# Kernel optimization log

Hardware: AMD Instinct MI355X
Metric: run time of the kernel (lower is better)

## Reference

```python
import jax, jax.numpy as jnp
import numpy as np

N_NODES = 50000
N_EDGES = 800000
F_IN = 128
F_OUT = 128


def gcn_conv(x, W, b, src, tgt, w, n):
    # x: [n, F_in]; GCNConv with add_self_loops=True, improved=False (fill=1.0)
    lin = x @ W  # [n, F_out]
    deg = jax.ops.segment_sum(w, tgt, num_segments=n) + 1.0  # self-loop weight 1
    dinv = jax.lax.rsqrt(deg)
    normw = dinv[src] * w * dinv[tgt]  # [E]
    agg = jax.ops.segment_sum(lin[src] * normw[:, None], tgt, num_segments=n)
    return agg + lin * (dinv * dinv)[:, None] + b


def setup_inputs() -> dict:
    key = jax.random.key(0)
    ks = jax.random.split(key, 16)
    X = jax.random.normal(ks[0], (1, N_NODES, F_IN), jnp.float32)
    edge_index = jax.random.randint(ks[1], (2, N_EDGES), 0, N_NODES, jnp.int64)
    edge_weight = jax.random.uniform(ks[2], (N_EDGES,), jnp.float32)
    H = jax.random.normal(ks[3], (1, N_NODES, F_OUT), jnp.float32)
    s = 1.0 / np.sqrt(F_IN)
    s2 = 1.0 / np.sqrt(2 * F_OUT)
    params = {
        'W_z': jax.random.uniform(ks[4], (F_IN, F_OUT), jnp.float32, -s, s),
        'b_z': jnp.zeros((F_OUT,), jnp.float32),
        'W_r': jax.random.uniform(ks[5], (F_IN, F_OUT), jnp.float32, -s, s),
        'b_r': jnp.zeros((F_OUT,), jnp.float32),
        'W_h': jax.random.uniform(ks[6], (F_IN, F_OUT), jnp.float32, -s, s),
        'b_h': jnp.zeros((F_OUT,), jnp.float32),
        'Wl_z': jax.random.uniform(ks[7], (2 * F_OUT, F_OUT), jnp.float32, -s2, s2),
        'bl_z': jax.random.uniform(ks[8], (F_OUT,), jnp.float32, -s2, s2),
        'Wl_r': jax.random.uniform(ks[9], (2 * F_OUT, F_OUT), jnp.float32, -s2, s2),
        'bl_r': jax.random.uniform(ks[10], (F_OUT,), jnp.float32, -s2, s2),
        'Wl_h': jax.random.uniform(ks[11], (2 * F_OUT, F_OUT), jnp.float32, -s2, s2),
        'bl_h': jax.random.uniform(ks[12], (F_OUT,), jnp.float32, -s2, s2),
    }
    return dict(X=X, edge_index=edge_index, edge_weight=edge_weight, H=H, **params)


def reference(X, edge_index, edge_weight, H,
              W_z, b_z, W_r, b_r, W_h, b_h,
              Wl_z, bl_z, Wl_r, bl_r, Wl_h, bl_h):
    B, N, _ = X.shape
    n = B * N
    x = X.reshape(n, -1)
    src, tgt = edge_index[0], edge_index[1]

    cz = gcn_conv(x, W_z, b_z, src, tgt, edge_weight, n).reshape(B, N, -1)
    Z = jax.nn.sigmoid(jnp.concatenate([cz, H], axis=2) @ Wl_z + bl_z)

    cr = gcn_conv(x, W_r, b_r, src, tgt, edge_weight, n).reshape(B, N, -1)
    R = jax.nn.sigmoid(jnp.concatenate([cr, H], axis=2) @ Wl_r + bl_r)

    ch = gcn_conv(x, W_h, b_h, src, tgt, edge_weight, n).reshape(B, N, -1)
    H_tilde = jnp.tanh(jnp.concatenate([ch, H * R], axis=2) @ Wl_h + bl_h)

    return Z * H + (1.0 - Z) * H_tilde
```

## Files before the change

kernel.cpp:

```cpp
#include <hip/hip_runtime.h>
#include <hip/hip_bf16.h>

#define N_NODES 50000
#define N_EDGES 800000
#define M_PAD   50048
#define NBLK5   1564
#define CAP     96

typedef __attribute__((ext_vector_type(8))) short bf16x8_t;
typedef __attribute__((ext_vector_type(4))) float f32x4_t;
typedef __attribute__((ext_vector_type(2))) float f32x2_t;

__device__ __forceinline__ unsigned short f2bf(float f) {
    unsigned u = __float_as_uint(f);
    u += 0x7FFFu + ((u >> 16) & 1u);
    return (unsigned short)(u >> 16);
}
__device__ __forceinline__ float bf2f(unsigned short h) {
    return __uint_as_float(((unsigned)h) << 16);
}


__global__ void prep1_kernel(const float* __restrict__ Wz, const float* __restrict__ Wr,
                             const float* __restrict__ Wh,
                             const float* __restrict__ bz, const float* __restrict__ br,
                             const float* __restrict__ bh,
                             const float* __restrict__ Wlz, const float* __restrict__ Wlr,
                             const float* __restrict__ Wlh,
                             const float* __restrict__ blz, const float* __restrict__ blr,
                             const float* __restrict__ blh,
                             float* __restrict__ Pf, float* __restrict__ cg,
                             int* __restrict__ counts) {
    int tid = blockIdx.x * 256 + threadIdx.x;
    if (tid < N_NODES) counts[tid] = 0;
    if (tid < 3 * 16384) {
        int g = tid / 16384, k = (tid / 128) % 128, n = tid & 127;
        const float* W  = (g == 0) ? Wz  : (g == 1) ? Wr  : Wh;
        const float* Wl = (g == 0) ? Wlz : (g == 1) ? Wlr : Wlh;
        float acc = 0.f;
        #pragma unroll 8
        for (int j = 0; j < 128; ++j)
            acc = fmaf(W[k * 128 + j], Wl[j * 128 + n], acc);
        Pf[tid] = acc;
    } else if (tid < 3 * 16384 + 384) {
        int u = tid - 3 * 16384;
        int g = u / 128, n = u & 127;
        const float* b  = (g == 0) ? bz  : (g == 1) ? br  : bh;
        const float* Wl = (g == 0) ? Wlz : (g == 1) ? Wlr : Wlh;
        const float* bl = (g == 0) ? blz : (g == 1) ? blr : blh;
        float acc = bl[n];
        #pragma unroll 8
        for (int j = 0; j < 128; ++j)
            acc = fmaf(b[j], Wl[j * 128 + n], acc);
        cg[u] = acc;
    }
}

__global__ void wfrag2_kernel(const float* __restrict__ Pf,
                              const float* __restrict__ Wlz, const float* __restrict__ Wlr,
                              const float* __restrict__ Wlh,
                              unsigned short* __restrict__ Wf2) {
    int tid = blockIdx.x * 256 + threadIdx.x;
    if (tid >= 6 * 2048) return;
    int m = tid / 2048, t = tid % 2048;
    int nt = t / 256, ks = (t / 64) % 4, lane = t % 64;
    const float* src;
    if (m < 3) src = Pf + m * 16384;
    else       src = ((m == 3) ? Wlz : (m == 4) ? Wlr : Wlh) + 128 * 128;
    unsigned short* dst = Wf2 + m * 16384 + ((nt * 4 + ks) * 64 + lane) * 8;
    int n = nt * 16 + (lane & 15);
    int k0 = ks * 32 + 8 * (lane >> 4);
    #pragma unroll
    for (int j = 0; j < 8; ++j) dst[j] = f2bf(src[(k0 + j) * 128 + n]);
}

__global__ void place_kernel(const int* __restrict__ EI, const float* __restrict__ EW,
                             int* __restrict__ counts, int2* __restrict__ rec,
                             const float* __restrict__ Hf, unsigned short* __restrict__ Hb) {
    int i = blockIdx.x * 256 + threadIdx.x;
    if (i < N_NODES * 32) {
        float4 h = ((const float4*)Hf)[i];
        ushort4 b;
        b.x = f2bf(h.x); b.y = f2bf(h.y); b.z = f2bf(h.z); b.w = f2bf(h.w);
        ((ushort4*)Hb)[i] = b;
    }
    if (i < N_EDGES) {
        int s = EI[i];
        int t = EI[N_EDGES + i];
        int pos = atomicAdd(&counts[t], 1);
        if (pos < CAP) rec[(size_t)t * CAP + pos] = make_int2(s, __float_as_int(EW[i]));
    }
}

__global__ void degconv_kernel(const int* __restrict__ counts, const int2* __restrict__ rec,
                               const float* __restrict__ X,
                               float* __restrict__ dinv, unsigned* __restrict__ Xf) {
    int tid = blockIdx.x * 256 + threadIdx.x;
    int node = tid >> 4;
    int j = tid & 15;
    if (node >= N_NODES) return;
    int c = counts[node]; c = (c < CAP) ? c : CAP;
    const int2* rb = rec + (size_t)node * CAP;
    float d = 0.f;
    for (int e = j; e < c; e += 16) d += __int_as_float(rb[e].y);
    d += __shfl_xor(d, 8, 16);
    d += __shfl_xor(d, 4, 16);
    d += __shfl_xor(d, 2, 16);
    d += __shfl_xor(d, 1, 16);
    d += 1.0f;
    float di = rsqrtf(d);
    if (j == 0) dinv[node] = di;
    float4 xa = *(const float4*)(X + (size_t)node * 128 + j * 8);
    float4 xb = *(const float4*)(X + (size_t)node * 128 + j * 8 + 4);
    float s0 = di * xa.x, s1 = di * xa.y, s2 = di * xa.z, s3 = di * xa.w;
    float s4 = di * xb.x, s5 = di * xb.y, s6 = di * xb.z, s7 = di * xb.w;
    int u0 = __builtin_amdgcn_cvt_pk_fp8_f32(s0, s1, 0, false);
    u0 = __builtin_amdgcn_cvt_pk_fp8_f32(s2, s3, u0, true);
    int u1 = __builtin_amdgcn_cvt_pk_fp8_f32(s4, s5, 0, false);
    u1 = __builtin_amdgcn_cvt_pk_fp8_f32(s6, s7, u1, true);
    uint2 o;
    o.x = (unsigned)u0; o.y = (unsigned)u1;
    *(uint2*)(Xf + (size_t)node * 32 + j * 2) = o;
}


__global__ __launch_bounds__(512) void fused_kernel(const unsigned* __restrict__ Xf,
                                                    const unsigned short* __restrict__ Hb,
                                                    const float* __restrict__ dinv,
                                                    const int* __restrict__ counts,
                                                    const int2* __restrict__ rec,
                                                    const unsigned short* __restrict__ Wf2,
                                                    const float* __restrict__ cg,
                                                    float* __restrict__ out) {
    __shared__ unsigned short ys[32][136];
    __shared__ unsigned short hs[32][136];
    __shared__ unsigned short rls[32][136];
    int tid = threadIdx.x;
    int wave = tid >> 6, lane = tid & 63;
    int rowbase = blockIdx.x * 32;
    int rlo = lane & 15;
    int kg = 8 * (lane >> 4);
    int n0 = wave;

    {
        int r = tid >> 4, co = (tid & 15) * 8;
        int row = rowbase + r;
        bf16x8_t h;
        if (row < N_NODES) h = *(const bf16x8_t*)(Hb + (size_t)row * 128 + co);
        else {
            #pragma unroll
            for (int j = 0; j < 8; ++j) h[j] = 0;
        }
        *(bf16x8_t*)(&hs[r][co]) = h;
    }

    {
        int nl = wave * 4 + (lane >> 4);
        int half = (lane >> 3) & 1;
        int lg = lane & 7;
        int node = rowbase + nl;
        float acc[16];
        #pragma unroll
        for (int j = 0; j < 16; ++j) acc[j] = 0.f;
        float dt = 0.f;
        if (node < N_NODES) {
            dt = dinv[node];
            if (half == 0) {
                uint4 xs = *(const uint4*)(Xf + (size_t)node * 32 + lg * 4);
                #pragma unroll
                for (int k = 0; k < 4; ++k) {
                    unsigned u = ((const unsigned*)&xs)[k];
                    f32x2_t lo = __builtin_amdgcn_cvt_pk_f32_fp8((int)u, false);
                    f32x2_t hi = __builtin_amdgcn_cvt_pk_f32_fp8((int)u, true);
                    acc[k * 4 + 0] = lo[0];
                    acc[k * 4 + 1] = lo[1];
                    acc[k * 4 + 2] = hi[0];
                    acc[k * 4 + 3] = hi[1];
                }
            }
            int c = counts[node]; c = (c < CAP) ? c : CAP;
            const int2* rb = rec + (size_t)node * CAP;
            int e = half;
            int2 r;
            uint4 xa;
            float wcur = 0.f;
            if (e < c) {
                r = rb[e];
                xa = *(const uint4*)(Xf + (size_t)r.x * 32 + lg * 4);
                wcur = __int_as_float(r.y);
                if (e + 2 < c) r = rb[e + 2];
            }
            while (e < c) {
                uint4 xn;
                float wn = 0.f;
                int en = e + 2;
                if (en < c) {
                    xn = *(const uint4*)(Xf + (size_t)r.x * 32 + lg * 4);
                    wn = __int_as_float(r.y);
                    if (en + 2 < c) r = rb[en + 2];
                }
                #pragma unroll
                for (int k = 0; k < 4; ++k) {
                    unsigned u = ((const unsigned*)&xa)[k];
                    f32x2_t lo = __builtin_amdgcn_cvt_pk_f32_fp8((int)u, false);
                    f32x2_t hi = __builtin_amdgcn_cvt_pk_f32_fp8((int)u, true);
                    acc[k * 4 + 0] = fmaf(wcur, lo[0], acc[k * 4 + 0]);
                    acc[k * 4 + 1] = fmaf(wcur, lo[1], acc[k * 4 + 1]);
                    acc[k * 4 + 2] = fmaf(wcur, hi[0], acc[k * 4 + 2]);
                    acc[k * 4 + 3] = fmaf(wcur, hi[1], acc[k * 4 + 3]);
                }
                xa = xn; wcur = wn;
                e = en;
            }
        }
        #pragma unroll
        for (int j = 0; j < 16; ++j) acc[j] += __shfl_xor(acc[j], 8, 64);
        if (half == 0) {
            ushort4 o0, o1, o2, o3;
            o0.x = f2bf(dt * acc[0]);  o0.y = f2bf(dt * acc[1]);
            o0.z = f2bf(dt * acc[2]);  o0.w = f2bf(dt * acc[3]);
            o1.x = f2bf(dt * acc[4]);  o1.y = f2bf(dt * acc[5]);
            o1.z = f2bf(dt * acc[6]);  o1.w = f2bf(dt * acc[7]);
            o2.x = f2bf(dt * acc[8]);  o2.y = f2bf(dt * acc[9]);
            o2.z = f2bf(dt * acc[10]); o2.w = f2bf(dt * acc[11]);
            o3.x = f2bf(dt * acc[12]); o3.y = f2bf(dt * acc[13]);
            o3.z = f2bf(dt * acc[14]); o3.w = f2bf(dt * acc[15]);
            *(ushort4*)(&ys[nl][lg * 16])      = o0;
            *(ushort4*)(&ys[nl][lg * 16 + 4])  = o1;
            *(ushort4*)(&ys[nl][lg * 16 + 8])  = o2;
            *(ushort4*)(&ys[nl][lg * 16 + 12]) = o3;
        }
    }
    __syncthreads();

    const unsigned short* Az = Wf2;
    const unsigned short* Ar = Wf2 + 16384;
    const unsigned short* Ah = Wf2 + 2 * 16384;
    const unsigned short* Bz = Wf2 + 3 * 16384;
    const unsigned short* Br = Wf2 + 4 * 16384;
    const unsigned short* Bh = Wf2 + 5 * 16384;
    int col = n0 * 16 + rlo;

    {
        f32x4_t a0 = f32x4_t{0.f, 0.f, 0.f, 0.f};
        f32x4_t a1 = f32x4_t{0.f, 0.f, 0.f, 0.f};
        #pragma unroll
        for (int ks = 0; ks < 4; ++ks) {
            bf16x8_t y0 = *(const bf16x8_t*)(&ys[rlo][ks * 32 + kg]);
            bf16x8_t y1 = *(const bf16x8_t*)(&ys[16 + rlo][ks * 32 + kg]);
            bf16x8_t b = *(const bf16x8_t*)(Ar + ((n0 * 4 + ks) * 64 + lane) * 8);
            a0 = __builtin_amdgcn_mfma_f32_16x16x32_bf16(y0, b, a0, 0, 0, 0);
            a1 = __builtin_amdgcn_mfma_f32_16x16x32_bf16(y1, b, a1, 0, 0, 0);
        }
        #pragma unroll
        for (int ks = 0; ks < 4; ++ks) {
            bf16x8_t h0 = *(const bf16x8_t*)(&hs[rlo][ks * 32 + kg]);
            bf16x8_t h1 = *(const bf16x8_t*)(&hs[16 + rlo][ks * 32 + kg]);
            bf16x8_t b = *(const bf16x8_t*)(Br + ((n0 * 4 + ks) * 64 + lane) * 8);
            a0 = __builtin_amdgcn_mfma_f32_16x16x32_bf16(h0, b, a0, 0, 0, 0);
            a1 = __builtin_amdgcn_mfma_f32_16x16x32_bf16(h1, b, a1, 0, 0, 0);
        }
        float crv = cg[128 + col];
        #pragma unroll
        for (int r = 0; r < 4; ++r) {
            float p0 = a0[r] + crv;
            float p1 = a1[r] + crv;
            rls[4 * (lane >> 4) + r][col] = f2bf(1.0f / (1.0f + __expf(-p0)));
            rls[16 + 4 * (lane >> 4) + r][col] = f2bf(1.0f / (1.0f + __expf(-p1)));
        }
    }
    __syncthreads();

    {
        f32x4_t az0 = f32x4_t{0.f, 0.f, 0.f, 0.f};
        f32x4_t az1 = f32x4_t{0.f, 0.f, 0.f, 0.f};
        f32x4_t at0 = f32x4_t{0.f, 0.f, 0.f, 0.f};
        f32x4_t at1 = f32x4_t{0.f, 0.f, 0.f, 0.f};
        #pragma unroll
        for (int ks = 0; ks < 4; ++ks) {
            bf16x8_t y0 = *(const bf16x8_t*)(&ys[rlo][ks * 32 + kg]);
            bf16x8_t y1 = *(const bf16x8_t*)(&ys[16 + rlo][ks * 32 + kg]);
            bf16x8_t bz_ = *(const bf16x8_t*)(Az + ((n0 * 4 + ks) * 64 + lane) * 8);
            bf16x8_t bh_ = *(const bf16x8_t*)(Ah + ((n0 * 4 + ks) * 64 + lane) * 8);
            az0 = __builtin_amdgcn_mfma_f32_16x16x32_bf16(y0, bz_, az0, 0, 0, 0);
            az1 = __builtin_amdgcn_mfma_f32_16x16x32_bf16(y1, bz_, az1, 0, 0, 0);
            at0 = __builtin_amdgcn_mfma_f32_16x16x32_bf16(y0, bh_, at0, 0, 0, 0);
            at1 = __builtin_amdgcn_mfma_f32_16x16x32_bf16(y1, bh_, at1, 0, 0, 0);
        }
        #pragma unroll
        for (int ks = 0; ks < 4; ++ks) {
            bf16x8_t h0 = *(const bf16x8_t*)(&hs[rlo][ks * 32 + kg]);
            bf16x8_t h1 = *(const bf16x8_t*)(&hs[16 + rlo][ks * 32 + kg]);
            bf16x8_t rf0 = *(const bf16x8_t*)(&rls[rlo][ks * 32 + kg]);
            bf16x8_t rf1 = *(const bf16x8_t*)(&rls[16 + rlo][ks * 32 + kg]);
            bf16x8_t hr0, hr1;
            #pragma unroll
            for (int j = 0; j < 8; ++j) {
                hr0[j] = (short)f2bf(bf2f((unsigned short)h0[j]) * bf2f((unsigned short)rf0[j]));
                hr1[j] = (short)f2bf(bf2f((unsigned short)h1[j]) * bf2f((unsigned short)rf1[j]));
            }
            bf16x8_t bz_ = *(const bf16x8_t*)(Bz + ((n0 * 4 + ks) * 64 + lane) * 8);
            bf16x8_t bh_ = *(const bf16x8_t*)(Bh + ((n0 * 4 + ks) * 64 + lane) * 8);
            az0 = __builtin_amdgcn_mfma_f32_16x16x32_bf16(h0, bz_, az0, 0, 0, 0);
            az1 = __builtin_amdgcn_mfma_f32_16x16x32_bf16(h1, bz_, az1, 0, 0, 0);
            at0 = __builtin_amdgcn_mfma_f32_16x16x32_bf16(hr0, bh_, at0, 0, 0, 0);
            at1 = __builtin_amdgcn_mfma_f32_16x16x32_bf16(hr1, bh_, at1, 0, 0, 0);
        }
        float czv = cg[col];
        float chv = cg[256 + col];
        #pragma unroll
        for (int rt = 0; rt < 2; ++rt) {
            #pragma unroll
            for (int r = 0; r < 4; ++r) {
                int rl = rt * 16 + 4 * (lane >> 4) + r;
                int row = rowbase + rl;
                if (row < N_NODES) {
                    float pz = (rt == 0 ? az0[r] : az1[r]) + czv;
                    float z = 1.0f / (1.0f + __expf(-pz));
                    float ph = (rt == 0 ? at0[r] : at1[r]) + chv;
                    float t = __expf(-2.0f * fabsf(ph));
                    float th = (1.0f - t) / (1.0f + t);
                    th = copysignf(th, ph);
                    float h = bf2f(hs[rl][col]);
                    out[(size_t)row * 128 + col] = z * h + (1.0f - z) * th;
                }
            }
        }
    }
}


extern "C" void kernel_launch(void* const* d_in, const int* in_sizes, int n_in,
                              void* d_out, int out_size, void* d_ws, size_t ws_size,
                              hipStream_t stream) {
    const float*      X   = (const float*)d_in[0];
    const int*        EI  = (const int*)d_in[1];
    const float*      EW  = (const float*)d_in[2];
    const float*      Hf  = (const float*)d_in[3];
    const float*      Wz  = (const float*)d_in[4];
    const float*      bz  = (const float*)d_in[5];
    const float*      Wr  = (const float*)d_in[6];
    const float*      br  = (const float*)d_in[7];
    const float*      Wh  = (const float*)d_in[8];
    const float*      bh  = (const float*)d_in[9];
    const float*      Wlz = (const float*)d_in[10];
    const float*      blz = (const float*)d_in[11];
    const float*      Wlr = (const float*)d_in[12];
    const float*      blr = (const float*)d_in[13];
    const float*      Wlh = (const float*)d_in[14];
    const float*      blh = (const float*)d_in[15];
    float* out = (float*)d_out;

    char* p = (char*)d_ws;
    auto alloc = [&](size_t bytes) {
        char* r = p;
        p += (bytes + 255) & ~(size_t)255;
        return r;
    };
    int*   counts = (int*)alloc(M_PAD * 4);
    float* dinv   = (float*)alloc(M_PAD * 4);
    int2*  rec    = (int2*)alloc((size_t)N_NODES * CAP * 8);
    unsigned*       Xf  = (unsigned*)alloc((size_t)M_PAD * 128);
    unsigned short* Hb  = (unsigned short*)alloc((size_t)M_PAD * 128 * 2);
    float* Pf  = (float*)alloc(3 * 128 * 128 * 4);
    float* cgb = (float*)alloc(3 * 128 * 4);
    unsigned short* Wf2 = (unsigned short*)alloc(6 * 128 * 128 * 2);

    prep1_kernel<<<196, 256, 0, stream>>>(Wz, Wr, Wh, bz, br, bh,
                                          Wlz, Wlr, Wlh, blz, blr, blh,
                                          Pf, cgb, counts);
    wfrag2_kernel<<<48, 256, 0, stream>>>(Pf, Wlz, Wlr, Wlh, Wf2);
    place_kernel<<<6250, 256, 0, stream>>>(EI, EW, counts, rec, Hf, Hb);
    degconv_kernel<<<3125, 256, 0, stream>>>(counts, rec, X, dinv, Xf);
    fused_kernel<<<NBLK5, 512, 0, stream>>>(Xf, Hb, dinv, counts, rec, Wf2, cgb, out);
}
```

Baseline: 124.0 us.

## Double fused kernel block to 1024 threads, four lane groups per node gather

The fused GCN-GRU kernel now runs 1024 threads per block. Each node's edge gather is split across four 8-lane groups instead of two, and the groups are combined with two xor-shuffles. In the MFMA stage each wave handles one 16-row tile instead of two, which halves per-wave accumulator and register use. The aim is more memory-level parallelism in the gather, which dominates the kernel. The cost is more shuffle reduction work and redundant weight-fragment loads, since the B fragments are now fetched by twice as many waves.

```diff
diff --git a/kernel.cpp b/kernel.cpp
--- a/kernel.cpp
+++ b/kernel.cpp
@@ -124,14 +124,14 @@
 }
 
 
-__global__ __launch_bounds__(512) void fused_kernel(const unsigned* __restrict__ Xf,
-                                                    const unsigned short* __restrict__ Hb,
-                                                    const float* __restrict__ dinv,
-                                                    const int* __restrict__ counts,
-                                                    const int2* __restrict__ rec,
-                                                    const unsigned short* __restrict__ Wf2,
-                                                    const float* __restrict__ cg,
-                                                    float* __restrict__ out) {
+__global__ __launch_bounds__(1024) void fused_kernel(const unsigned* __restrict__ Xf,
+                                                     const unsigned short* __restrict__ Hb,
+                                                     const float* __restrict__ dinv,
+                                                     const int* __restrict__ counts,
+                                                     const int2* __restrict__ rec,
+                                                     const unsigned short* __restrict__ Wf2,
+                                                     const float* __restrict__ cg,
+                                                     float* __restrict__ out) {
     __shared__ unsigned short ys[32][136];
     __shared__ unsigned short hs[32][136];
     __shared__ unsigned short rls[32][136];
@@ -140,23 +140,21 @@
     int rowbase = blockIdx.x * 32;
     int rlo = lane & 15;
     int kg = 8 * (lane >> 4);
-    int n0 = wave;
+    int n0 = wave & 7;
+    int rt = wave >> 3;
 
     {
-        int r = tid >> 4, co = (tid & 15) * 8;
+        int r = tid >> 5, co = (tid & 31) * 4;
         int row = rowbase + r;
-        bf16x8_t h;
-        if (row < N_NODES) h = *(const bf16x8_t*)(Hb + (size_t)row * 128 + co);
-        else {
-            #pragma unroll
-            for (int j = 0; j < 8; ++j) h[j] = 0;
-        }
-        *(bf16x8_t*)(&hs[r][co]) = h;
+        ushort4 h;
+        if (row < N_NODES) h = *(const ushort4*)(Hb + (size_t)row * 128 + co);
+        else { h.x = 0; h.y = 0; h.z = 0; h.w = 0; }
+        *(ushort4*)(&hs[r][co]) = h;
     }
 
     {
-        int nl = wave * 4 + (lane >> 4);
-        int half = (lane >> 3) & 1;
+        int nl = 2 * wave + (lane >> 5);
+        int grp = (lane >> 3) & 3;
         int lg = lane & 7;
         int node = rowbase + nl;
         float acc[16];
@@ -165,7 +163,7 @@
         float dt = 0.f;
         if (node < N_NODES) {
             dt = dinv[node];
-            if (half == 0) {
+            if (grp == 0) {
                 uint4 xs = *(const uint4*)(Xf + (size_t)node * 32 + lg * 4);
                 #pragma unroll
                 for (int k = 0; k < 4; ++k) {
@@ -180,7 +178,7 @@
             }
             int c = counts[node]; c = (c < CAP) ? c : CAP;
             const int2* rb = rec + (size_t)node * CAP;
-            int e = half;
+            int e = grp;
             int2 r;
             uint4 xa;
             float wcur = 0.f;
@@ -188,16 +186,16 @@
                 r = rb[e];
                 xa = *(const uint4*)(Xf + (size_t)r.x * 32 + lg * 4);
                 wcur = __int_as_float(r.y);
-                if (e + 2 < c) r = rb[e + 2];
+                if (e + 4 < c) r = rb[e + 4];
             }
             while (e < c) {
                 uint4 xn;
                 float wn = 0.f;
-                int en = e + 2;
+                int en = e + 4;
                 if (en < c) {
                     xn = *(const uint4*)(Xf + (size_t)r.x * 32 + lg * 4);
                     wn = __int_as_float(r.y);
-                    if (en + 2 < c) r = rb[en + 2];
+                    if (en + 4 < c) r = rb[en + 4];
                 }
                 #pragma unroll
                 for (int k = 0; k < 4; ++k) {
@@ -214,8 +212,13 @@
             }
         }
         #pragma unroll
-        for (int j = 0; j < 16; ++j) acc[j] += __shfl_xor(acc[j], 8, 64);
-        if (half == 0) {
+        for (int j = 0; j < 16; ++j) {
+            float v = acc[j];
+            v += __shfl_xor(v, 8, 64);
+            v += __shfl_xor(v, 16, 64);
+            acc[j] = v;
+        }
+        if (grp == 0) {
             ushort4 o0, o1, o2, o3;
             o0.x = f2bf(dt * acc[0]);  o0.y = f2bf(dt * acc[1]);
             o0.z = f2bf(dt * acc[2]);  o0.w = f2bf(dt * acc[3]);
@@ -240,90 +243,70 @@
     const unsigned short* Br = Wf2 + 4 * 16384;
     const unsigned short* Bh = Wf2 + 5 * 16384;
     int col = n0 * 16 + rlo;
+    int yrow = rt * 16 + rlo;
 
     {
-        f32x4_t a0 = f32x4_t{0.f, 0.f, 0.f, 0.f};
-        f32x4_t a1 = f32x4_t{0.f, 0.f, 0.f, 0.f};
+        f32x4_t a = f32x4_t{0.f, 0.f, 0.f, 0.f};
         #pragma unroll
         for (int ks = 0; ks < 4; ++ks) {
-            bf16x8_t y0 = *(const bf16x8_t*)(&ys[rlo][ks * 32 + kg]);
-            bf16x8_t y1 = *(const bf16x8_t*)(&ys[16 + rlo][ks * 32 + kg]);
+            bf16x8_t y = *(const bf16x8_t*)(&ys[yrow][ks * 32 + kg]);
             bf16x8_t b = *(const bf16x8_t*)(Ar + ((n0 * 4 + ks) * 64 + lane) * 8);
-            a0 = __builtin_amdgcn_mfma_f32_16x16x32_bf16(y0, b, a0, 0, 0, 0);
-            a1 = __builtin_amdgcn_mfma_f32_16x16x32_bf16(y1, b, a1, 0, 0, 0);
+            a = __builtin_amdgcn_mfma_f32_16x16x32_bf16(y, b, a, 0, 0, 0);
         }
         #pragma unroll
         for (int ks = 0; ks < 4; ++ks) {
-            bf16x8_t h0 = *(const bf16x8_t*)(&hs[rlo][ks * 32 + kg]);
-            bf16x8_t h1 = *(const bf16x8_t*)(&hs[16 + rlo][ks * 32 + kg]);
+            bf16x8_t h = *(const bf16x8_t*)(&hs[yrow][ks * 32 + kg]);
             bf16x8_t b = *(const bf16x8_t*)(Br + ((n0 * 4 + ks) * 64 + lane) * 8);
-            a0 = __builtin_amdgcn_mfma_f32_16x16x32_bf16(h0, b, a0, 0, 0, 0);
-            a1 = __builtin_amdgcn_mfma_f32_16x16x32_bf16(h1, b, a1, 0, 0, 0);
+            a = __builtin_amdgcn_mfma_f32_16x16x32_bf16(h, b, a, 0, 0, 0);
         }
         float crv = cg[128 + col];
         #pragma unroll
         for (int r = 0; r < 4; ++r) {
-            float p0 = a0[r] + crv;
-            float p1 = a1[r] + crv;
-            rls[4 * (lane >> 4) + r][col] = f2bf(1.0f / (1.0f + __expf(-p0)));
-            rls[16 + 4 * (lane >> 4) + r][col] = f2bf(1.0f / (1.0f + __expf(-p1)));
+            float pv = a[r] + crv;
+            rls[rt * 16 + 4 * (lane >> 4) + r][col] = f2bf(1.0f / (1.0f + __expf(-pv)));
         }
     }
     __syncthreads();
 
     {
-        f32x4_t az0 = f32x4_t{0.f, 0.f, 0.f, 0.f};
-        f32x4_t az1 = f32x4_t{0.f, 0.f, 0.f, 0.f};
-        f32x4_t at0 = f32x4_t{0.f, 0.f, 0.f, 0.f};
-        f32x4_t at1 = f32x4_t{0.f, 0.f, 0.f, 0.f};
+        f32x4_t az = f32x4_t{0.f, 0.f, 0.f, 0.f};
+        f32x4_t at = f32x4_t{0.f, 0.f, 0.f, 0.f};
         #pragma unroll
         for (int ks = 0; ks < 4; ++ks) {
-            bf16x8_t y0 = *(const bf16x8_t*)(&ys[rlo][ks * 32 + kg]);
-            bf16x8_t y1 = *(const bf16x8_t*)(&ys[16 + rlo][ks * 32 + kg]);
+            bf16x8_t y = *(const bf16x8_t*)(&ys[yrow][ks * 32 + kg]);
             bf16x8_t bz_ = *(const bf16x8_t*)(Az + ((n0 * 4 + ks) * 64 + lane) * 8);
             bf16x8_t bh_ = *(const bf16x8_t*)(Ah + ((n0 * 4 + ks) * 64 + lane) * 8);
-            az0 = __builtin_amdgcn_mfma_f32_16x16x32_bf16(y0, bz_, az0, 0, 0, 0);
-            az1 = __builtin_amdgcn_mfma_f32_16x16x32_bf16(y1, bz_, az1, 0, 0, 0);
-            at0 = __builtin_amdgcn_mfma_f32_16x16x32_bf16(y0, bh_, at0, 0, 0, 0);
-            at1 = __builtin_amdgcn_mfma_f32_16x16x32_bf16(y1, bh_, at1, 0, 0, 0);
+            az = __builtin_amdgcn_mfma_f32_16x16x32_bf16(y, bz_, az, 0, 0, 0);
+            at = __builtin_amdgcn_mfma_f32_16x16x32_bf16(y, bh_, at, 0, 0, 0);
         }
         #pragma unroll
         for (int ks = 0; ks < 4; ++ks) {
-            bf16x8_t h0 = *(const bf16x8_t*)(&hs[rlo][ks * 32 + kg]);
-            bf16x8_t h1 = *(const bf16x8_t*)(&hs[16 + rlo][ks * 32 + kg]);
-            bf16x8_t rf0 = *(const bf16x8_t*)(&rls[rlo][ks * 32 + kg]);
-            bf16x8_t rf1 = *(const bf16x8_t*)(&rls[16 + rlo][ks * 32 + kg]);
-            bf16x8_t hr0, hr1;
+            bf16x8_t h = *(const bf16x8_t*)(&hs[yrow][ks * 32 + kg]);
+            bf16x8_t rf = *(const bf16x8_t*)(&rls[yrow][ks * 32 + kg]);
+            bf16x8_t hr;
             #pragma unroll
-            for (int j = 0; j < 8; ++j) {
-                hr0[j] = (short)f2bf(bf2f((unsigned short)h0[j]) * bf2f((unsigned short)rf0[j]));
-                hr1[j] = (short)f2bf(bf2f((unsigned short)h1[j]) * bf2f((unsigned short)rf1[j]));
-            }
+            for (int j = 0; j < 8; ++j)
+                hr[j] = (short)f2bf(bf2f((unsigned short)h[j]) * bf2f((unsigned short)rf[j]));
             bf16x8_t bz_ = *(const bf16x8_t*)(Bz + ((n0 * 4 + ks) * 64 + lane) * 8);
             bf16x8_t bh_ = *(const bf16x8_t*)(Bh + ((n0 * 4 + ks) * 64 + lane) * 8);
-            az0 = __builtin_amdgcn_mfma_f32_16x16x32_bf16(h0, bz_, az0, 0, 0, 0);
-            az1 = __builtin_amdgcn_mfma_f32_16x16x32_bf16(h1, bz_, az1, 0, 0, 0);
-            at0 = __builtin_amdgcn_mfma_f32_16x16x32_bf16(hr0, bh_, at0, 0, 0, 0);
-            at1 = __builtin_amdgcn_mfma_f32_16x16x32_bf16(hr1, bh_, at1, 0, 0, 0);
+            az = __builtin_amdgcn_mfma_f32_16x16x32_bf16(h, bz_, az, 0, 0, 0);
+            at = __builtin_amdgcn_mfma_f32_16x16x32_bf16(hr, bh_, at, 0, 0, 0);
         }
         float czv = cg[col];
         float chv = cg[256 + col];
         #pragma unroll
-        for (int rt = 0; rt < 2; ++rt) {
-            #pragma unroll
-            for (int r = 0; r < 4; ++r) {
-                int rl = rt * 16 + 4 * (lane >> 4) + r;
-                int row = rowbase + rl;
-                if (row < N_NODES) {
-                    float pz = (rt == 0 ? az0[r] : az1[r]) + czv;
-                    float z = 1.0f / (1.0f + __expf(-pz));
-                    float ph = (rt == 0 ? at0[r] : at1[r]) + chv;
-                    float t = __expf(-2.0f * fabsf(ph));
-                    float th = (1.0f - t) / (1.0f + t);
-                    th = copysignf(th, ph);
-                    float h = bf2f(hs[rl][col]);
-                    out[(size_t)row * 128 + col] = z * h + (1.0f - z) * th;
-                }
+        for (int r = 0; r < 4; ++r) {
+            int rl = rt * 16 + 4 * (lane >> 4) + r;
+            int row = rowbase + rl;
+            if (row < N_NODES) {
+                float pz = az[r] + czv;
+                float z = 1.0f / (1.0f + __expf(-pz));
+                float ph = at[r] + chv;
+                float t = __expf(-2.0f * fabsf(ph));
+                float th = (1.0f - t) / (1.0f + t);
+                th = copysignf(th, ph);
+                float h = bf2f(hs[rl][col]);
+                out[(size_t)row * 128 + col] = z * h + (1.0f - z) * th;
             }
         }
     }
@@ -372,5 +355,5 @@
     wfrag2_kernel<<<48, 256, 0, stream>>>(Pf, Wlz, Wlr, Wlh, Wf2);
     place_kernel<<<6250, 256, 0, stream>>>(EI, EW, counts, rec, Hf, Hb);
     degconv_kernel<<<3125, 256, 0, stream>>>(counts, rec, X, dinv, Xf);
-    fused_kernel<<<NBLK5, 512, 0, stream>>>(Xf, Hb, dinv, counts, rec, Wf2, cgb, out);
-}
+    fused_kernel<<<NBLK5, 1024, 0, stream>>>(Xf, Hb, dinv, counts, rec, Wf2, cgb, out);
+}
```

Result: slower. 127.0 us (+2.4%).
